# Optimization experiments

Hardware: AMD Instinct MI355X
Metric: run time of the kernel (lower is better)

Reference implementation:

```python
import jax, jax.numpy as jnp
import numpy as np


def _conv(x, w, pad):
    return jax.lax.conv_general_dilated(
        x, w, (1, 1), [(pad, pad), (pad, pad)],
        dimension_numbers=('NCHW', 'OIHW', 'NCHW'))


def _avgpool2(x):
    B, C, H, W = x.shape
    return x.reshape(B, C, H // 2, 2, W // 2, 2).mean(axis=(3, 5))


def setup_inputs() -> dict:
    key = jax.random.key(0)
    ks = jax.random.split(key, 10)
    B = 1024
    x = jax.random.uniform(ks[0], (B, 1, 28, 28), jnp.float32)
    # depthwise-separable conv params (in=1 -> depthwise is a plain 3x3 conv)
    dw_w = jax.random.normal(ks[1], (1, 1, 3, 3), jnp.float32) * 0.3
    pw_w = jax.random.normal(ks[2], (32, 1, 1, 1), jnp.float32) * 0.3
    pw_b = jax.random.normal(ks[3], (32,), jnp.float32) * 0.05
    # fixed 4-qubit entangling unitary (real orthogonal 16x16), stand-in for tq.RandomLayer(n_ops=8)
    U = jnp.asarray(np.linalg.qr(np.random.default_rng(0).standard_normal((16, 16)))[0],
                    jnp.float32)
    fus_w = jax.random.normal(ks[4], (128, 36, 3, 3), jnp.float32) * (1.0 / np.sqrt(36 * 9))
    fus_b = jax.random.normal(ks[5], (128,), jnp.float32) * 0.05
    F = 128 * 7 * 7
    cls_w = jax.random.normal(ks[6], (10, F), jnp.float32) * (1.0 / np.sqrt(F))
    cls_b = jax.random.normal(ks[7], (10,), jnp.float32) * 0.05
    reg_w = jax.random.normal(ks[8], (1, F), jnp.float32) * (1.0 / np.sqrt(F))
    reg_b = jax.random.normal(ks[9], (1,), jnp.float32) * 0.05
    return {'x': x, 'dw_w': dw_w, 'pw_w': pw_w, 'pw_b': pw_b, 'U': U,
            'fus_w': fus_w, 'fus_b': fus_b, 'cls_w': cls_w, 'cls_b': cls_b,
            'reg_w': reg_w, 'reg_b': reg_b}


def _quantum_patches(x, U):
    # x: (B,1,28,28) -> 14x14 grid of 2x2 patches, 4 RY angles per patch
    B = x.shape[0]
    p = x.reshape(B, 14, 2, 14, 2).transpose(0, 1, 3, 2, 4).reshape(B, 14, 14, 4)
    h = 0.5 * p
    a = jnp.stack([jnp.cos(h), jnp.sin(h)], axis=-1)       # (B,14,14,4,2)
    # RY-encoded product state |psi> = kron over 4 wires -> 16 real amplitudes
    amp = jnp.einsum('...i,...j,...k,...l->...ijkl',
                     a[..., 0, :], a[..., 1, :], a[..., 2, :], a[..., 3, :]
                     ).reshape(B, 14, 14, 16)
    state = amp @ U.T                                       # entangling layer
    probs = state * state
    idx = jnp.arange(16)
    # PauliZ expectation per wire; wire 0 is the most significant bit
    signs = 1.0 - 2.0 * (((idx[None, :] >> (3 - jnp.arange(4)[:, None])) & 1)
                         .astype(jnp.float32))              # (4,16)
    meas = probs @ signs.T                                  # (B,14,14,4)
    # replicate torch.cat(patches,dim=1).view(B,4,14,14): flat row-major then reshape
    return meas.reshape(B, 14 * 14 * 4).reshape(B, 4, 14, 14)


def reference(x, dw_w, pw_w, pw_b, U, fus_w, fus_b, cls_w, cls_b, reg_w, reg_b):
    B = x.shape[0]
    out_ds = _conv(_conv(x, dw_w, 1), pw_w, 0) + pw_b[None, :, None, None]  # (B,32,28,28)
    out_q = _quantum_patches(x, U)                                          # (B,4,14,14)
    out = jnp.concatenate([_avgpool2(out_ds), out_q], axis=1)               # (B,36,14,14)
    out = jax.nn.relu(_conv(out, fus_w, 1) + fus_b[None, :, None, None])    # (B,128,14,14)
    out = _avgpool2(out)                                                    # (B,128,7,7)
    flat = out.reshape(B, -1)
    logits = flat @ cls_w.T + cls_b
    aux = flat @ reg_w.T + reg_b
    return (logits, aux)
```

## Files before the change

### kernel.cpp

```cpp
#include <hip/hip_runtime.h>
#include <math.h>


typedef __bf16 bf16x8 __attribute__((ext_vector_type(8)));
typedef float  f32x16 __attribute__((ext_vector_type(16)));

union Pack8 { __bf16 h[8]; uint4 v; };

__global__ __launch_bounds__(256) void prep(
    const float* __restrict__ fus_w,
    const float* __restrict__ cls_w,
    const float* __restrict__ reg_w,
    __bf16* __restrict__ bfrag,
    float* __restrict__ clsTT)
{
    const int gid = blockIdx.x * 256 + threadIdx.x;
    if (gid < 55296) {
        const int j    = gid & 7;
        const int frag = gid >> 3;
        const int lane = frag & 63;
        const int rest = frag >> 6;
        const int m  = rest % 27;
        const int nt = rest / 27;
        const int t  = m / 3, ks = m - t * 3;
        const int n  = nt * 32 + (lane & 31);
        const int ic = ks * 16 + (lane >> 5) * 8 + j;
        const float v = (ic < 36) ? fus_w[n * 324 + ic * 9 + t] : 0.f;
        bfrag[gid] = (__bf16)v;
    } else if (gid < 55296 + 68992) {
        const int g2 = gid - 55296;
        const int k  = g2 / 6272;
        const int f  = g2 - k * 6272;
        const float v = (k < 10) ? cls_w[g2] : reg_w[f];
        const int oc   = f / 49;
        const int cell = f - oc * 49;
        const int nt = oc >> 5, l31 = oc & 31;
        const int mt = cell >> 3, r = cell & 7, q = r >> 1, hk = r & 1;
        clsTT[((((k * 4 + nt) * 7 + mt) * 4 + q) * 2 + hk) * 32 + l31] = v;
    } else if (gid < 55296 + 68992 + 9856) {
        const int g3  = gid - 55296 - 68992;
        const int k   = g3 / 896;
        const int rem = g3 - k * 896;
        const int oc  = rem / 7;
        const int cell = 49 + (rem - oc * 7);
        const int nt = oc >> 5, l31 = oc & 31;
        const int mt = cell >> 3, r = cell & 7, q = r >> 1, hk = r & 1;
        clsTT[((((k * 4 + nt) * 7 + mt) * 4 + q) * 2 + hk) * 32 + l31] = 0.f;
    }
}

__global__ __launch_bounds__(256, 3) void quanv_fused(
    const float* __restrict__ x,
    const float* __restrict__ dw_w,
    const float* __restrict__ pw_w,
    const float* __restrict__ pw_b,
    const float* __restrict__ U,
    const __bf16* __restrict__ bfrag,
    const float* __restrict__ fus_b,
    const float* __restrict__ clsTT,
    const float* __restrict__ cls_b,
    const float* __restrict__ reg_b,
    float* __restrict__ out,
    int B)
{
    __shared__ __align__(16) __bf16 actT[256 * 48];
    __shared__ float xs[784];
    __shared__ float red[48];

    const int b   = blockIdx.x;
    const int tid = threadIdx.x;
    const float* xb = x + b * 784;

    {
        uint4 z; z.x = 0; z.y = 0; z.z = 0; z.w = 0;
        for (int i = tid; i < 1536; i += 256) ((uint4*)actT)[i] = z;
        for (int i = tid; i < 784; i += 256) xs[i] = xb[i];
    }
    __syncthreads();

    if (tid < 196) {
        const int i = tid / 14, j = tid % 14;
        const int Y = 2 * i, X = 2 * j;

        float w9[9];
        #pragma unroll
        for (int t = 0; t < 9; ++t) w9[t] = dw_w[t];
        float dsum = 0.f;
        #pragma unroll
        for (int dy = 0; dy < 2; ++dy) {
            #pragma unroll
            for (int dx = 0; dx < 2; ++dx) {
                const int cy = Y + dy, cx = X + dx;
                #pragma unroll
                for (int ky = 0; ky < 3; ++ky) {
                    const int yy = cy + ky - 1;
                    if (yy < 0 || yy > 27) continue;
                    #pragma unroll
                    for (int kx = 0; kx < 3; ++kx) {
                        const int xx = cx + kx - 1;
                        if (xx < 0 || xx > 27) continue;
                        dsum += xs[yy * 28 + xx] * w9[ky * 3 + kx];
                    }
                }
            }
        }
        const float dpool = 0.25f * dsum;

        const int sp_o  = (i + 1) * 16 + (j + 1);
        const int rot_o = (i + 1) % 6;
        #pragma unroll
        for (int c8 = 0; c8 < 4; ++c8) {
            Pack8 pk;
            #pragma unroll
            for (int e = 0; e < 8; ++e)
                pk.h[e] = (__bf16)(pw_w[c8 * 8 + e] * dpool + pw_b[c8 * 8 + e]);
            int slot = c8 + rot_o; if (slot >= 6) slot -= 6;
            ((uint4*)actT)[sp_o * 6 + slot] = pk.v;
        }

        const float p0 = xs[Y * 28 + X],       p1 = xs[Y * 28 + X + 1];
        const float p2 = xs[(Y + 1) * 28 + X], p3 = xs[(Y + 1) * 28 + X + 1];
        float c0, s0, c1, s1, c2, s2, c3, s3;
        sincosf(0.5f * p0, &s0, &c0);
        sincosf(0.5f * p1, &s1, &c1);
        sincosf(0.5f * p2, &s2, &c2);
        sincosf(0.5f * p3, &s3, &c3);
        float a01[4] = {c0 * c1, c0 * s1, s0 * c1, s0 * s1};
        float a23[4] = {c2 * c3, c2 * s3, s2 * c3, s2 * s3};
        float amp[16];
        #pragma unroll
        for (int hi = 0; hi < 4; ++hi)
            #pragma unroll
            for (int lo = 0; lo < 4; ++lo)
                amp[hi * 4 + lo] = a01[hi] * a23[lo];

        float meas[4] = {0.f, 0.f, 0.f, 0.f};
        #pragma unroll
        for (int m = 0; m < 16; ++m) {
            float st = 0.f;
            #pragma unroll
            for (int n = 0; n < 16; ++n) st = fmaf(U[m * 16 + n], amp[n], st);
            const float pm = st * st;
            meas[0] += ((m >> 3) & 1) ? -pm : pm;
            meas[1] += ((m >> 2) & 1) ? -pm : pm;
            meas[2] += ((m >> 1) & 1) ? -pm : pm;
            meas[3] += (m & 1) ? -pm : pm;
        }
        const int fbase = i * 56 + j * 4;
        #pragma unroll
        for (int w = 0; w < 4; ++w) {
            const int f  = fbase + w;
            const int ch = f / 196;
            const int sp = f - ch * 196;
            const int r2 = sp / 14 + 1, c2i = sp % 14 + 1;
            const int sp2 = r2 * 16 + c2i;
            int slot = 4 + r2 % 6; if (slot >= 6) slot -= 6;
            actT[sp2 * 48 + slot * 8 + ch] = (__bf16)meas[w];
        }
    }
    __syncthreads();

    const int lane = tid & 63, nt = tid >> 6;
    const int l31  = lane & 31, hk = lane >> 5;
    const float fb_l = fus_b[nt * 32 + l31];

    bf16x8 bfr[27];
    {
        const bf16x8* __restrict__ bp = ((const bf16x8*)bfrag) + (nt * 27 * 64 + lane);
        #pragma unroll
        for (int m = 0; m < 27; ++m) bfr[m] = bp[m * 64];
    }

    float a11[11];
    #pragma unroll
    for (int k = 0; k < 11; ++k) a11[k] = 0.f;

    for (int mt = 0; mt < 7; ++mt) {
        const int mp   = mt * 32 + l31;
        int cell = mp >> 2;
        const int cc = (cell < 49) ? cell : 48;
        const int py = (cc * 9363) >> 16;
        const int px = cc - py * 7;
        const int yy = 2 * py + ((mp >> 1) & 1);
        const int xx = 2 * px + (mp & 1);
        const int rowbase = yy * 16 + xx;
        const int ym6 = yy - 6 * ((yy * 43) >> 8);

        f32x16 acc = {0.f,0.f,0.f,0.f,0.f,0.f,0.f,0.f,
                      0.f,0.f,0.f,0.f,0.f,0.f,0.f,0.f};

        #pragma unroll
        for (int t = 0; t < 9; ++t) {
            const int ky = t / 3, kx = t - ky * 3;
            int rot = ym6 + ky; if (rot >= 6) rot -= 6;
            const int row = rowbase + ky * 16 + kx;
            #pragma unroll
            for (int ks = 0; ks < 3; ++ks) {
                int slot = 2 * ks + hk + rot; if (slot >= 6) slot -= 6;
                const bf16x8 af = *(const bf16x8*)(actT + row * 48 + slot * 8);
                acc = __builtin_amdgcn_mfma_f32_32x32x16_bf16(af, bfr[t * 3 + ks],
                                                              acc, 0, 0, 0);
            }
        }

        #pragma unroll
        for (int q = 0; q < 4; ++q) {
            float pv = 0.f;
            #pragma unroll
            for (int s = 0; s < 4; ++s) {
                const float v = acc[q * 4 + s] + fb_l;
                pv += (v > 0.f ? v : 0.f);
            }
            pv *= 0.25f;
            const float* cw = clsTT + (((nt * 7 + mt) * 4 + q) * 2 + hk) * 32 + l31;
            #pragma unroll
            for (int k = 0; k < 11; ++k)
                a11[k] = fmaf(pv, cw[k * 7168], a11[k]);
        }
    }
    __syncthreads();

    const int wv = tid >> 6;
    #pragma unroll
    for (int k = 0; k < 11; ++k) {
        float a = a11[k];
        #pragma unroll
        for (int off = 32; off > 0; off >>= 1) a += __shfl_down(a, off, 64);
        if (lane == 0) red[k * 4 + wv] = a;
    }
    __syncthreads();
    if (tid < 11) {
        const float v = red[tid * 4] + red[tid * 4 + 1] + red[tid * 4 + 2] + red[tid * 4 + 3];
        if (tid < 10) out[b * 10 + tid] = v + cls_b[tid];
        else          out[B * 10 + b]   = v + reg_b[0];
    }
}

extern "C" void kernel_launch(void* const* d_in, const int* in_sizes, int n_in,
                              void* d_out, int out_size, void* d_ws, size_t ws_size,
                              hipStream_t stream) {
    const float* x    = (const float*)d_in[0];
    const float* dw_w = (const float*)d_in[1];
    const float* pw_w = (const float*)d_in[2];
    const float* pw_b = (const float*)d_in[3];
    const float* U    = (const float*)d_in[4];
    const float* fw   = (const float*)d_in[5];
    const float* fb   = (const float*)d_in[6];
    const float* cw   = (const float*)d_in[7];
    const float* cb   = (const float*)d_in[8];
    const float* rw   = (const float*)d_in[9];
    const float* rb   = (const float*)d_in[10];
    const int B = in_sizes[0] / 784;

    __bf16* bfrag = (__bf16*)d_ws;
    float*  clsTT = (float*)((char*)d_ws + 110592);

    prep<<<(55296 + 68992 + 9856 + 255) / 256, 256, 0, stream>>>(fw, cw, rw, bfrag, clsTT);
    quanv_fused<<<B, 256, 0, stream>>>(x, dw_w, pw_w, pw_b, U, bfrag, fb,
                                       clsTT, cb, rb, (float*)d_out, B);
}
```

Measured before the change: 123.4 us.

## Pad activation rows to 56 and interleave classifier weights for float4 loads

The LDS activation tile goes from a 48-element rotated-slot layout to a plain 56-element padded row stride. This removes the per-load modulo-6 slot arithmetic and relies on the padding to avoid bank conflicts. The classifier/regressor weights are re-laid out so each lane's 11 outputs sit contiguously, padded to 12. That turns eleven strided scalar loads into three float4 loads per pooled value. LDS use grows slightly, which could affect occupancy.

```diff
diff --git a/kernel.cpp b/kernel.cpp
--- a/kernel.cpp
+++ b/kernel.cpp
@@ -27,25 +27,26 @@
         const int ic = ks * 16 + (lane >> 5) * 8 + j;
         const float v = (ic < 36) ? fus_w[n * 324 + ic * 9 + t] : 0.f;
         bfrag[gid] = (__bf16)v;
-    } else if (gid < 55296 + 68992) {
-        const int g2 = gid - 55296;
-        const int k  = g2 / 6272;
-        const int f  = g2 - k * 6272;
-        const float v = (k < 10) ? cls_w[g2] : reg_w[f];
-        const int oc   = f / 49;
-        const int cell = f - oc * 49;
-        const int nt = oc >> 5, l31 = oc & 31;
-        const int mt = cell >> 3, r = cell & 7, q = r >> 1, hk = r & 1;
-        clsTT[((((k * 4 + nt) * 7 + mt) * 4 + q) * 2 + hk) * 32 + l31] = v;
-    } else if (gid < 55296 + 68992 + 9856) {
-        const int g3  = gid - 55296 - 68992;
-        const int k   = g3 / 896;
-        const int rem = g3 - k * 896;
-        const int oc  = rem / 7;
-        const int cell = 49 + (rem - oc * 7);
-        const int nt = oc >> 5, l31 = oc & 31;
-        const int mt = cell >> 3, r = cell & 7, q = r >> 1, hk = r & 1;
-        clsTT[((((k * 4 + nt) * 7 + mt) * 4 + q) * 2 + hk) * 32 + l31] = 0.f;
+    } else if (gid < 55296 + 86016) {
+        const int e   = gid - 55296;
+        const int kk  = e % 12;
+        const int r0  = e / 12;
+        const int l31 = r0 & 31;
+        const int r1  = r0 >> 5;
+        const int hk  = r1 & 1;
+        const int r2  = r1 >> 1;
+        const int q   = r2 & 3;
+        const int r3  = r2 >> 2;
+        const int mt  = r3 % 7;
+        const int nt  = r3 / 7;
+        const int oc   = nt * 32 + l31;
+        const int cell = mt * 8 + q * 2 + hk;
+        float v = 0.f;
+        if (cell < 49 && kk < 11) {
+            const int f = oc * 49 + cell;
+            v = (kk < 10) ? cls_w[kk * 6272 + f] : reg_w[f];
+        }
+        clsTT[e] = v;
     }
 }
 
@@ -63,7 +64,7 @@
     float* __restrict__ out,
     int B)
 {
-    __shared__ __align__(16) __bf16 actT[256 * 48];
+    __shared__ __align__(16) __bf16 actT[256 * 56];
     __shared__ float xs[784];
     __shared__ float red[48];
 
@@ -73,7 +74,7 @@
 
     {
         uint4 z; z.x = 0; z.y = 0; z.z = 0; z.w = 0;
-        for (int i = tid; i < 1536; i += 256) ((uint4*)actT)[i] = z;
+        for (int i = tid; i < 1792; i += 256) ((uint4*)actT)[i] = z;
         for (int i = tid; i < 784; i += 256) xs[i] = xb[i];
     }
     __syncthreads();
@@ -106,16 +107,14 @@
         }
         const float dpool = 0.25f * dsum;
 
-        const int sp_o  = (i + 1) * 16 + (j + 1);
-        const int rot_o = (i + 1) % 6;
+        const int sp_o = (i + 1) * 16 + (j + 1);
         #pragma unroll
         for (int c8 = 0; c8 < 4; ++c8) {
             Pack8 pk;
             #pragma unroll
             for (int e = 0; e < 8; ++e)
                 pk.h[e] = (__bf16)(pw_w[c8 * 8 + e] * dpool + pw_b[c8 * 8 + e]);
-            int slot = c8 + rot_o; if (slot >= 6) slot -= 6;
-            ((uint4*)actT)[sp_o * 6 + slot] = pk.v;
+            ((uint4*)actT)[sp_o * 7 + c8] = pk.v;
         }
 
         const float p0 = xs[Y * 28 + X],       p1 = xs[Y * 28 + X + 1];
@@ -154,8 +153,7 @@
             const int sp = f - ch * 196;
             const int r2 = sp / 14 + 1, c2i = sp % 14 + 1;
             const int sp2 = r2 * 16 + c2i;
-            int slot = 4 + r2 % 6; if (slot >= 6) slot -= 6;
-            actT[sp2 * 48 + slot * 8 + ch] = (__bf16)meas[w];
+            actT[sp2 * 56 + 32 + ch] = (__bf16)meas[w];
         }
     }
     __syncthreads();
@@ -174,6 +172,9 @@
     float a11[11];
     #pragma unroll
     for (int k = 0; k < 11; ++k) a11[k] = 0.f;
+
+    const float4* __restrict__ cls4 =
+        ((const float4*)clsTT) + ((((nt * 7) * 4) * 2 + hk) * 32 + l31) * 3;
 
     for (int mt = 0; mt < 7; ++mt) {
         const int mp   = mt * 32 + l31;
@@ -184,7 +185,6 @@
         const int yy = 2 * py + ((mp >> 1) & 1);
         const int xx = 2 * px + (mp & 1);
         const int rowbase = yy * 16 + xx;
-        const int ym6 = yy - 6 * ((yy * 43) >> 8);
 
         f32x16 acc = {0.f,0.f,0.f,0.f,0.f,0.f,0.f,0.f,
                       0.f,0.f,0.f,0.f,0.f,0.f,0.f,0.f};
@@ -192,17 +192,17 @@
         #pragma unroll
         for (int t = 0; t < 9; ++t) {
             const int ky = t / 3, kx = t - ky * 3;
-            int rot = ym6 + ky; if (rot >= 6) rot -= 6;
             const int row = rowbase + ky * 16 + kx;
+            const __bf16* rp = actT + row * 56 + hk * 8;
             #pragma unroll
             for (int ks = 0; ks < 3; ++ks) {
-                int slot = 2 * ks + hk + rot; if (slot >= 6) slot -= 6;
-                const bf16x8 af = *(const bf16x8*)(actT + row * 48 + slot * 8);
+                const bf16x8 af = *(const bf16x8*)(rp + ks * 16);
                 acc = __builtin_amdgcn_mfma_f32_32x32x16_bf16(af, bfr[t * 3 + ks],
                                                               acc, 0, 0, 0);
             }
         }
 
+        const float4* cwm = cls4 + mt * (4 * 2 * 32 * 3);
         #pragma unroll
         for (int q = 0; q < 4; ++q) {
             float pv = 0.f;
@@ -212,10 +212,20 @@
                 pv += (v > 0.f ? v : 0.f);
             }
             pv *= 0.25f;
-            const float* cw = clsTT + (((nt * 7 + mt) * 4 + q) * 2 + hk) * 32 + l31;
-            #pragma unroll
-            for (int k = 0; k < 11; ++k)
-                a11[k] = fmaf(pv, cw[k * 7168], a11[k]);
+            const float4 w0 = cwm[q * 192 + 0];
+            const float4 w1 = cwm[q * 192 + 1];
+            const float4 w2 = cwm[q * 192 + 2];
+            a11[0]  = fmaf(pv, w0.x, a11[0]);
+            a11[1]  = fmaf(pv, w0.y, a11[1]);
+            a11[2]  = fmaf(pv, w0.z, a11[2]);
+            a11[3]  = fmaf(pv, w0.w, a11[3]);
+            a11[4]  = fmaf(pv, w1.x, a11[4]);
+            a11[5]  = fmaf(pv, w1.y, a11[5]);
+            a11[6]  = fmaf(pv, w1.z, a11[6]);
+            a11[7]  = fmaf(pv, w1.w, a11[7]);
+            a11[8]  = fmaf(pv, w2.x, a11[8]);
+            a11[9]  = fmaf(pv, w2.y, a11[9]);
+            a11[10] = fmaf(pv, w2.z, a11[10]);
         }
     }
     __syncthreads();
@@ -255,7 +265,7 @@
     __bf16* bfrag = (__bf16*)d_ws;
     float*  clsTT = (float*)((char*)d_ws + 110592);
 
-    prep<<<(55296 + 68992 + 9856 + 255) / 256, 256, 0, stream>>>(fw, cw, rw, bfrag, clsTT);
+    prep<<<(55296 + 86016 + 255) / 256, 256, 0, stream>>>(fw, cw, rw, bfrag, clsTT);
     quanv_fused<<<B, 256, 0, stream>>>(x, dw_w, pw_w, pw_b, U, bfrag, fb,
                                        clsTT, cb, rb, (float*)d_out, B);
 }
```

Result: no change. 122.3 us (-1.0%).
